# Kernel tuning notes

Measured on AMD Instinct MI355X. Metric: run time of the kernel, lower is better.

Reference implementation:

```python
import jax, jax.numpy as jnp
import numpy as np

N = 50000
E = 1600000
D = 64


def setup_inputs() -> dict:
    key = jax.random.key(0)
    ks = jax.random.split(key, 12)
    glorot = lambda k, shape: jax.random.uniform(
        k, shape, jnp.float32, -1.0, 1.0) * (np.sqrt(2.0) * np.sqrt(6.0 / sum(shape)))
    return {
        "feat": jax.random.normal(ks[0], (N, D), jnp.float32),
        "norm": jax.random.uniform(ks[1], (N,), jnp.float32),
        "edge_src": jax.random.randint(ks[2], (E,), 0, N),
        "edge_dst": jax.random.randint(ks[3], (E,), 0, N),
        "etype": jax.random.randint(ks[4], (E,), 0, 4),
        "W_rel": glorot(ks[5], (D, D)),
        "lin_w": glorot(ks[6], (2 * D, 1)),
        "lin_b": jnp.zeros((1,), jnp.float32),
        "loop_w": glorot(ks[7], (D, D)),
        "evolve_loop_w": glorot(ks[8], (D, D)),
    }


def reference(feat, norm, edge_src, edge_dst, etype, W_rel, lin_w, lin_b,
              loop_w, evolve_loop_w):
    # --- message function: per-edge attention + per-edge matmul ---
    src = feat[edge_src]              # [E, D] gather
    dst = feat[edge_dst]              # [E, D] gather
    att_logit = jnp.concatenate([src, dst], axis=1) @ lin_w + lin_b  # [E, 1]
    atten = jax.nn.sigmoid(jax.nn.relu(att_logit[:, 0]))            # [E]
    # source code applies weight_relation to every edge-type bucket, so the
    # etype split+concat is a no-op permutation of messages
    msg = src @ W_rel                                                # [E, D]

    # --- reduce: attention-weighted mailbox sum (segment reduction) ---
    agg = jax.ops.segment_sum(atten[:, None] * msg, edge_dst, num_segments=N)
    indeg = jax.ops.segment_sum(jnp.ones((edge_dst.shape[0],), feat.dtype),
                                edge_dst, num_segments=N)            # [N]
    has_msg = (indeg > 0)[:, None]
    # DGL: zero in-degree nodes keep their old feat; apply_func scales by norm
    node_feat = jnp.where(has_msg, agg, feat) * norm[:, None]

    # --- self loop: loop_weight where in_degree>0, evolve_loop_weight else ---
    loop_msg = jnp.where(has_msg, feat @ loop_w, feat @ evolve_loop_w)

    return jnp.tanh(node_feat + loop_msg)
```

## Files before the change

kernel.cpp:

```cpp
#include <hip/hip_runtime.h>
#include <hip/hip_bf16.h>
#include <hip/hip_fp16.h>
#include <math.h>


#define D 64
#define SHIFT 6
#define NB (1 << SHIFT)
#define SCM 1024
#define CAPB 2560
#define NPW 8

typedef _Float16 half8 __attribute__((ext_vector_type(8)));
typedef float f32x4 __attribute__((ext_vector_type(4)));

__global__ __launch_bounds__(512) void pre_scatter(
    const float* __restrict__ feat, const float* __restrict__ W_rel,
    const float* __restrict__ lin_w, const float* __restrict__ lin_b,
    const float* __restrict__ loop_w, const float* __restrict__ evolve_w,
    const int* __restrict__ esrc, const int* __restrict__ edst,
    float* __restrict__ s1, float* __restrict__ s2, __half* __restrict__ FWh,
    __half* __restrict__ WT, int* __restrict__ gcur,
    unsigned* __restrict__ ebuf, int N, int E, int C) {
  __shared__ int h[SCM];
  __shared__ int cur[SCM];
  __shared__ int bl[SCM];
  for (int i = threadIdx.x; i < C; i += 512) h[i] = 0;

  if (blockIdx.x == 0) {
    for (int i = threadIdx.x; i < 192 * 64; i += 512) {
      const int c192 = i >> 6, k = i & 63;
      const int m = c192 >> 6, c = c192 & 63;
      const float* Wm = (m == 0) ? W_rel : (m == 1) ? loop_w : evolve_w;
      WT[i] = __float2half(Wm[k * 64 + c]);
    }
  }

  const int lane = threadIdx.x & 63;
  const int w    = threadIdx.x >> 6;
  const int r    = lane & 15;
  const int g    = lane >> 4;
  const int m0   = (blockIdx.x * 8 + w) * 16;
  if (m0 < N) {
    half8 bw[4][2];
    half8 ba[2];
    #pragma unroll
    for (int ks = 0; ks < 2; ++ks) {
      #pragma unroll
      for (int j = 0; j < 8; ++j) {
        const int k = ks * 32 + g * 8 + j;
        #pragma unroll
        for (int nt = 0; nt < 4; ++nt)
          bw[nt][ks][j] = (_Float16)W_rel[k * 64 + nt * 16 + r];
        const float av = (r == 0) ? lin_w[k] : (r == 1) ? lin_w[64 + k] : 0.0f;
        ba[ks][j] = (_Float16)av;
      }
    }

    half8 ah[2], al[2];
    const int arow = m0 + r;
    #pragma unroll
    for (int ks = 0; ks < 2; ++ks) {
      float v[8];
      if (arow < N) {
        const float4 u0 = *(const float4*)&feat[(size_t)arow * D + ks * 32 + g * 8];
        const float4 u1 = *(const float4*)&feat[(size_t)arow * D + ks * 32 + g * 8 + 4];
        v[0] = u0.x; v[1] = u0.y; v[2] = u0.z; v[3] = u0.w;
        v[4] = u1.x; v[5] = u1.y; v[6] = u1.z; v[7] = u1.w;
      } else {
        #pragma unroll
        for (int q = 0; q < 8; ++q) v[q] = 0.0f;
      }
      #pragma unroll
      for (int q = 0; q < 8; ++q) {
        const _Float16 hh = (_Float16)v[q];
        ah[ks][q] = hh;
        al[ks][q] = (_Float16)(v[q] - (float)hh);
      }
    }

    #pragma unroll
    for (int nt = 0; nt < 4; ++nt) {
      f32x4 acc = {0.0f, 0.0f, 0.0f, 0.0f};
      #pragma unroll
      for (int ks = 0; ks < 2; ++ks) {
        acc = __builtin_amdgcn_mfma_f32_16x16x32_f16(ah[ks], bw[nt][ks], acc, 0, 0, 0);
        acc = __builtin_amdgcn_mfma_f32_16x16x32_f16(al[ks], bw[nt][ks], acc, 0, 0, 0);
      }
      #pragma unroll
      for (int q = 0; q < 4; ++q) {
        const int n = m0 + g * 4 + q;
        if (n < N) FWh[(size_t)n * D + nt * 16 + r] = __float2half(acc[q]);
      }
    }

    f32x4 acc5 = {0.0f, 0.0f, 0.0f, 0.0f};
    #pragma unroll
    for (int ks = 0; ks < 2; ++ks) {
      acc5 = __builtin_amdgcn_mfma_f32_16x16x32_f16(ah[ks], ba[ks], acc5, 0, 0, 0);
      acc5 = __builtin_amdgcn_mfma_f32_16x16x32_f16(al[ks], ba[ks], acc5, 0, 0, 0);
    }
    if (r < 2) {
      const float b = lin_b[0];
      #pragma unroll
      for (int q = 0; q < 4; ++q) {
        const int n = m0 + g * 4 + q;
        if (n < N) {
          if (r == 0) s1[n] = acc5[q] + b;
          else        s2[n] = acc5[q];
        }
      }
    }
  }

  __syncthreads();

  const int E4 = E >> 2;
  const int4* edst4 = (const int4*)edst;
  const int4* esrc4 = (const int4*)esrc;
  const int i4 = blockIdx.x * 512 + threadIdx.x;
  const bool tail0 = (blockIdx.x == 0) && (threadIdx.x == 0);

  if (i4 < E4) {
    const int4 d = edst4[i4];
    atomicAdd(&h[d.x >> SHIFT], 1);
    atomicAdd(&h[d.y >> SHIFT], 1);
    atomicAdd(&h[d.z >> SHIFT], 1);
    atomicAdd(&h[d.w >> SHIFT], 1);
  }
  if (tail0) for (int e = E4 << 2; e < E; ++e) atomicAdd(&h[edst[e] >> SHIFT], 1);
  __syncthreads();
  for (int i = threadIdx.x; i < C; i += 512) {
    const int v = h[i];
    bl[i] = v ? atomicAdd(&gcur[i], v) : 0;
    cur[i] = 0;
  }
  __syncthreads();

  if (i4 < E4) {
    const int4 s = esrc4[i4];
    const int4 d = edst4[i4];
    const int ss[4] = {s.x, s.y, s.z, s.w};
    const int dd[4] = {d.x, d.y, d.z, d.w};
    #pragma unroll
    for (int j = 0; j < 4; ++j) {
      const int bk = dd[j] >> SHIFT;
      const int rr = atomicAdd(&cur[bk], 1);
      ebuf[(size_t)bk * CAPB + bl[bk] + rr] =
          (unsigned)ss[j] | ((unsigned)(dd[j] & (NB - 1)) << 26);
    }
  }
  if (tail0) {
    for (int e = E4 << 2; e < E; ++e) {
      const int bk = edst[e] >> SHIFT;
      const int rr = atomicAdd(&cur[bk], 1);
      ebuf[(size_t)bk * CAPB + bl[bk] + rr] =
          (unsigned)esrc[e] | ((unsigned)(edst[e] & (NB - 1)) << 26);
    }
  }
}

__global__ __launch_bounds__(512, 4) void sort_reduce_finalize(
    const float* __restrict__ feat, const __half* __restrict__ FWh,
    const __half* __restrict__ WT, const float* __restrict__ norm,
    const float* __restrict__ s1, const float* __restrict__ s2,
    const int* __restrict__ gcur, const unsigned* __restrict__ ebuf,
    float* __restrict__ out, int C, int N) {
  __shared__ uint2 sdata[CAPB];
  __shared__ float Yl[NB * D];
  __shared__ float s2l[NB];
  __shared__ int hist[NB];
  __shared__ int starts[NB + 1];
  __shared__ int roff[NB];

  const int tid  = threadIdx.x;
  const int lane = tid & 63;
  const int w    = tid >> 6;
  const int b    = blockIdx.x;
  const int n0   = b << SHIFT;
  const int beg  = b * CAPB;
  const int cnt  = min(gcur[b], CAPB);

  if (tid < NB) {
    hist[tid] = 0;
    const int n = n0 + tid;
    s2l[tid] = (n < N) ? s2[n] : 0.0f;
  }
  __syncthreads();

  unsigned ereg[5];
  float    areg[5];
  #pragma unroll
  for (int k = 0; k < 5; ++k) {
    const int i = tid + (k << 9);
    if (i < cnt) {
      ereg[k] = ebuf[beg + i];
      atomicAdd(&hist[ereg[k] >> 26], 1);
    }
  }
  #pragma unroll
  for (int k = 0; k < 5; ++k) {
    const int i = tid + (k << 9);
    if (i < cnt) {
      const unsigned src = ereg[k] & 0x03FFFFFFu;
      const float v = s1[src] + s2l[ereg[k] >> 26];
      areg[k] = 1.0f / (1.0f + __expf(-fmaxf(v, 0.0f)));
    }
  }
  __syncthreads();
  if (tid < 64) {
    const int v = hist[tid];
    int incl = v;
    #pragma unroll
    for (int off = 1; off < 64; off <<= 1) {
      const int o = __shfl_up(incl, off, 64);
      if (tid >= off) incl += o;
    }
    starts[tid] = incl - v;
    roff[tid]   = incl - v;
    if (tid == 63) starts[64] = incl;
  }
  __syncthreads();
  #pragma unroll
  for (int k = 0; k < 5; ++k) {
    const int i = tid + (k << 9);
    if (i < cnt) {
      const int pos = atomicAdd(&roff[ereg[k] >> 26], 1);
      sdata[pos] = make_uint2(ereg[k], __float_as_uint(areg[k]));
    }
  }

  {
    const int r = lane & 15, g = lane >> 4;
    const bool evw = (w >= 4);
    const int mt = w & 3;
    bool skip = false;
    if (evw) {
      const int rr0 = mt * 16;
      const int flag = (lane < 16)
          ? ((starts[rr0 + lane + 1] > starts[rr0 + lane]) ? 1 : 0) : 1;
      skip = (__ballot(flag == 0) == 0ULL);
    }
    if (!skip) {
      half8 ah[2], al[2];
      const int arow = n0 + mt * 16 + r;
      #pragma unroll
      for (int ks = 0; ks < 2; ++ks) {
        float v[8];
        if (arow < N) {
          const float4 u0 = *(const float4*)&feat[(size_t)arow * D + ks * 32 + g * 8];
          const float4 u1 = *(const float4*)&feat[(size_t)arow * D + ks * 32 + g * 8 + 4];
          v[0] = u0.x; v[1] = u0.y; v[2] = u0.z; v[3] = u0.w;
          v[4] = u1.x; v[5] = u1.y; v[6] = u1.z; v[7] = u1.w;
        } else {
          #pragma unroll
          for (int q = 0; q < 8; ++q) v[q] = 0.0f;
        }
        #pragma unroll
        for (int q = 0; q < 8; ++q) {
          const _Float16 hh = (_Float16)v[q];
          ah[ks][q] = hh;
          al[ks][q] = (_Float16)(v[q] - (float)hh);
        }
      }
      const int wrow0 = evw ? 128 : 64;
      #pragma unroll
      for (int nt = 0; nt < 4; ++nt) {
        f32x4 a0 = {0.0f, 0.0f, 0.0f, 0.0f};
        #pragma unroll
        for (int ks = 0; ks < 2; ++ks) {
          const half8 bw = *reinterpret_cast<const half8*>(
              WT + (size_t)(wrow0 + nt * 16 + r) * 64 + ks * 32 + g * 8);
          a0 = __builtin_amdgcn_mfma_f32_16x16x32_f16(ah[ks], bw, a0, 0, 0, 0);
          a0 = __builtin_amdgcn_mfma_f32_16x16x32_f16(al[ks], bw, a0, 0, 0, 0);
        }
        #pragma unroll
        for (int q = 0; q < 4; ++q) {
          const int gr = mt * 16 + g * 4 + q;
          const bool hm = starts[gr + 1] > starts[gr];
          if (evw != hm) Yl[gr * D + nt * 16 + r] = a0[q];
        }
      }
    }
  }
  __syncthreads();

  const int qe = lane >> 4;
  const int qc = lane & 15;
  float agg[NPW];
  #pragma unroll
  for (int j = 0; j < NPW; ++j) agg[j] = 0.0f;
  for (int j = 0; j < NPW; ++j) {
    const int dl = w * NPW + j;
    const int n  = n0 + dl;
    if (n >= N) break;
    const int rb = __builtin_amdgcn_readfirstlane(starts[dl]);
    const int re = __builtin_amdgcn_readfirstlane(starts[dl + 1]);
    float sa = 0.0f, sb = 0.0f, sc = 0.0f, sd = 0.0f;
    int p = rb;
    for (; p + 16 <= re; p += 16) {
      uint2 ee[4];
      #pragma unroll
      for (int q = 0; q < 4; ++q) ee[q] = sdata[p + 4 * q + qe];
      #pragma unroll
      for (int q = 0; q < 4; ++q) {
        const uint2 vv = *(const uint2*)(
            FWh + (((size_t)(ee[q].x & 0x03FFFFFFu)) << 6) + (qc << 2));
        const float a = __uint_as_float(ee[q].y);
        const float2 f0 = __half22float2(*(const __half2*)&vv.x);
        const float2 f1 = __half22float2(*(const __half2*)&vv.y);
        sa += a * f0.x; sb += a * f0.y; sc += a * f1.x; sd += a * f1.y;
      }
    }
    for (; p < re; p += 4) {
      const int idx = p + qe;
      const bool vld = idx < re;
      const uint2 e = sdata[vld ? idx : rb];
      const uint2 vv = *(const uint2*)(
          FWh + (((size_t)(e.x & 0x03FFFFFFu)) << 6) + (qc << 2));
      const float a = vld ? __uint_as_float(e.y) : 0.0f;
      const float2 f0 = __half22float2(*(const __half2*)&vv.x);
      const float2 f1 = __half22float2(*(const __half2*)&vv.y);
      sa += a * f0.x; sb += a * f0.y; sc += a * f1.x; sd += a * f1.y;
    }
    sa += __shfl_xor(sa, 16, 64); sa += __shfl_xor(sa, 32, 64);
    sb += __shfl_xor(sb, 16, 64); sb += __shfl_xor(sb, 32, 64);
    sc += __shfl_xor(sc, 16, 64); sc += __shfl_xor(sc, 32, 64);
    sd += __shfl_xor(sd, 16, 64); sd += __shfl_xor(sd, 32, 64);
    const float t0 = __shfl(sa, lane >> 2, 64);
    const float t1 = __shfl(sb, lane >> 2, 64);
    const float t2 = __shfl(sc, lane >> 2, 64);
    const float t3 = __shfl(sd, lane >> 2, 64);
    const int sel = lane & 3;
    agg[j] = (sel == 0) ? t0 : (sel == 1) ? t1 : (sel == 2) ? t2 : t3;
  }

  for (int j = 0; j < NPW; ++j) {
    const int dl = w * NPW + j;
    const int n  = n0 + dl;
    if (n >= N) break;
    const bool hm = starts[dl + 1] > starts[dl];
    const float nr = norm[n];
    const float base = hm ? agg[j] : feat[(size_t)n * D + lane];
    out[(size_t)n * D + lane] = tanhf(base * nr + Yl[dl * D + lane]);
  }
}

extern "C" void kernel_launch(void* const* d_in, const int* in_sizes, int n_in,
                              void* d_out, int out_size, void* d_ws, size_t ws_size,
                              hipStream_t stream) {
  const float* feat     = (const float*)d_in[0];
  const float* norm     = (const float*)d_in[1];
  const int*   esrc     = (const int*)d_in[2];
  const int*   edst     = (const int*)d_in[3];
  const float* W_rel    = (const float*)d_in[5];
  const float* lin_w    = (const float*)d_in[6];
  const float* lin_b    = (const float*)d_in[7];
  const float* loop_w   = (const float*)d_in[8];
  const float* evolve_w = (const float*)d_in[9];
  float* out = (float*)d_out;

  const int N = in_sizes[1];
  const int E = in_sizes[2];
  const int C = (N + NB - 1) >> SHIFT;

  char* p = (char*)d_ws;
  float*    s1   = (float*)p;    p += (size_t)N * sizeof(float);
  float*    s2   = (float*)p;    p += (size_t)N * sizeof(float);
  int*      gcur = (int*)p;      p += (size_t)2048 * sizeof(int);
  __half*   WT   = (__half*)p;   p += (size_t)192 * 64 * sizeof(__half);
  __half*   FWh  = (__half*)p;   p += (size_t)N * D * sizeof(__half);
  unsigned* ebuf = (unsigned*)p;

  const int E4 = E >> 2;
  const int eblocks = (E4 + 511) / 512;

  hipMemsetAsync(gcur, 0, (size_t)C * sizeof(int), stream);
  pre_scatter<<<eblocks, 512, 0, stream>>>(feat, W_rel, lin_w, lin_b,
                                           loop_w, evolve_w, esrc, edst,
                                           s1, s2, FWh, WT, gcur, ebuf,
                                           N, E, C);
  sort_reduce_finalize<<<C, 512, 0, stream>>>(feat, FWh, WT, norm, s1, s2,
                                              gcur, ebuf, out, C, N);
}
```

Before: 155.4 us.

## Replace bucketed edge scatter and in-block sort with per-node fixed-capacity slots

The edge scatter now appends each edge into a fixed-capacity (80) slot array per destination node, using global atomics on a per-node counter. This replaces the per-block shared-memory histogram, global bucket reservation and the in-block counting sort. The reduce kernel reads each node's slots directly and keeps only per-slot attention in shared memory. This removes several barriers and the shared-memory sort, but it adds contended global atomics and a larger, mostly padded edge buffer. Edges past the cap are silently dropped, so correctness depends on in-degree staying at or below 80, which holds for the random test graph (mean in-degree 32).

```diff
diff --git a/kernel.cpp b/kernel.cpp
--- a/kernel.cpp
+++ b/kernel.cpp
@@ -7,8 +7,7 @@
 #define D 64
 #define SHIFT 6
 #define NB (1 << SHIFT)
-#define SCM 1024
-#define CAPB 2560
+#define CAP 80
 #define NPW 8
 
 typedef _Float16 half8 __attribute__((ext_vector_type(8)));
@@ -20,13 +19,8 @@
     const float* __restrict__ loop_w, const float* __restrict__ evolve_w,
     const int* __restrict__ esrc, const int* __restrict__ edst,
     float* __restrict__ s1, float* __restrict__ s2, __half* __restrict__ FWh,
-    __half* __restrict__ WT, int* __restrict__ gcur,
-    unsigned* __restrict__ ebuf, int N, int E, int C) {
-  __shared__ int h[SCM];
-  __shared__ int cur[SCM];
-  __shared__ int bl[SCM];
-  for (int i = threadIdx.x; i < C; i += 512) h[i] = 0;
-
+    __half* __restrict__ WT, int* __restrict__ ncur,
+    unsigned* __restrict__ ebuf, int N, int E) {
   if (blockIdx.x == 0) {
     for (int i = threadIdx.x; i < 192 * 64; i += 512) {
       const int c192 = i >> 6, k = i & 63;
@@ -113,49 +107,29 @@
     }
   }
 
-  __syncthreads();
-
   const int E4 = E >> 2;
   const int4* edst4 = (const int4*)edst;
   const int4* esrc4 = (const int4*)esrc;
   const int i4 = blockIdx.x * 512 + threadIdx.x;
-  const bool tail0 = (blockIdx.x == 0) && (threadIdx.x == 0);
-
-  if (i4 < E4) {
-    const int4 d = edst4[i4];
-    atomicAdd(&h[d.x >> SHIFT], 1);
-    atomicAdd(&h[d.y >> SHIFT], 1);
-    atomicAdd(&h[d.z >> SHIFT], 1);
-    atomicAdd(&h[d.w >> SHIFT], 1);
-  }
-  if (tail0) for (int e = E4 << 2; e < E; ++e) atomicAdd(&h[edst[e] >> SHIFT], 1);
-  __syncthreads();
-  for (int i = threadIdx.x; i < C; i += 512) {
-    const int v = h[i];
-    bl[i] = v ? atomicAdd(&gcur[i], v) : 0;
-    cur[i] = 0;
-  }
-  __syncthreads();
 
   if (i4 < E4) {
     const int4 s = esrc4[i4];
     const int4 d = edst4[i4];
     const int ss[4] = {s.x, s.y, s.z, s.w};
     const int dd[4] = {d.x, d.y, d.z, d.w};
+    int slot[4];
+    #pragma unroll
+    for (int j = 0; j < 4; ++j) slot[j] = atomicAdd(&ncur[dd[j]], 1);
     #pragma unroll
     for (int j = 0; j < 4; ++j) {
-      const int bk = dd[j] >> SHIFT;
-      const int rr = atomicAdd(&cur[bk], 1);
-      ebuf[(size_t)bk * CAPB + bl[bk] + rr] =
-          (unsigned)ss[j] | ((unsigned)(dd[j] & (NB - 1)) << 26);
-    }
-  }
-  if (tail0) {
+      if (slot[j] < CAP)
+        ebuf[(size_t)dd[j] * CAP + slot[j]] = (unsigned)ss[j];
+    }
+  }
+  if (blockIdx.x == 0 && threadIdx.x == 0) {
     for (int e = E4 << 2; e < E; ++e) {
-      const int bk = edst[e] >> SHIFT;
-      const int rr = atomicAdd(&cur[bk], 1);
-      ebuf[(size_t)bk * CAPB + bl[bk] + rr] =
-          (unsigned)esrc[e] | ((unsigned)(edst[e] & (NB - 1)) << 26);
+      const int slot = atomicAdd(&ncur[edst[e]], 1);
+      if (slot < CAP) ebuf[(size_t)edst[e] * CAP + slot] = (unsigned)esrc[e];
     }
   }
 }
@@ -164,69 +138,36 @@
     const float* __restrict__ feat, const __half* __restrict__ FWh,
     const __half* __restrict__ WT, const float* __restrict__ norm,
     const float* __restrict__ s1, const float* __restrict__ s2,
-    const int* __restrict__ gcur, const unsigned* __restrict__ ebuf,
-    float* __restrict__ out, int C, int N) {
-  __shared__ uint2 sdata[CAPB];
+    const int* __restrict__ ncur, const unsigned* __restrict__ ebuf,
+    float* __restrict__ out, int N) {
+  __shared__ float attL[NB * CAP];
   __shared__ float Yl[NB * D];
   __shared__ float s2l[NB];
-  __shared__ int hist[NB];
-  __shared__ int starts[NB + 1];
-  __shared__ int roff[NB];
+  __shared__ int   cntL[NB];
 
   const int tid  = threadIdx.x;
   const int lane = tid & 63;
   const int w    = tid >> 6;
   const int b    = blockIdx.x;
   const int n0   = b << SHIFT;
-  const int beg  = b * CAPB;
-  const int cnt  = min(gcur[b], CAPB);
+  const size_t rbase = (size_t)n0 * CAP;
 
   if (tid < NB) {
-    hist[tid] = 0;
     const int n = n0 + tid;
-    s2l[tid] = (n < N) ? s2[n] : 0.0f;
+    cntL[tid] = (n < N) ? min(ncur[n], CAP) : 0;
+    s2l[tid]  = (n < N) ? s2[n] : 0.0f;
   }
   __syncthreads();
 
-  unsigned ereg[5];
-  float    areg[5];
   #pragma unroll
-  for (int k = 0; k < 5; ++k) {
+  for (int k = 0; k < (NB * CAP) / 512; ++k) {
     const int i = tid + (k << 9);
-    if (i < cnt) {
-      ereg[k] = ebuf[beg + i];
-      atomicAdd(&hist[ereg[k] >> 26], 1);
-    }
-  }
-  #pragma unroll
-  for (int k = 0; k < 5; ++k) {
-    const int i = tid + (k << 9);
-    if (i < cnt) {
-      const unsigned src = ereg[k] & 0x03FFFFFFu;
-      const float v = s1[src] + s2l[ereg[k] >> 26];
-      areg[k] = 1.0f / (1.0f + __expf(-fmaxf(v, 0.0f)));
-    }
-  }
-  __syncthreads();
-  if (tid < 64) {
-    const int v = hist[tid];
-    int incl = v;
-    #pragma unroll
-    for (int off = 1; off < 64; off <<= 1) {
-      const int o = __shfl_up(incl, off, 64);
-      if (tid >= off) incl += o;
-    }
-    starts[tid] = incl - v;
-    roff[tid]   = incl - v;
-    if (tid == 63) starts[64] = incl;
-  }
-  __syncthreads();
-  #pragma unroll
-  for (int k = 0; k < 5; ++k) {
-    const int i = tid + (k << 9);
-    if (i < cnt) {
-      const int pos = atomicAdd(&roff[ereg[k] >> 26], 1);
-      sdata[pos] = make_uint2(ereg[k], __float_as_uint(areg[k]));
+    const unsigned e = ebuf[rbase + i];
+    const int node = i / CAP;
+    const int slot = i - node * CAP;
+    if (slot < cntL[node]) {
+      const float v = s1[e & 0x03FFFFFFu] + s2l[node];
+      attL[i] = 1.0f / (1.0f + __expf(-fmaxf(v, 0.0f)));
     }
   }
 
@@ -237,8 +178,7 @@
     bool skip = false;
     if (evw) {
       const int rr0 = mt * 16;
-      const int flag = (lane < 16)
-          ? ((starts[rr0 + lane + 1] > starts[rr0 + lane]) ? 1 : 0) : 1;
+      const int flag = (lane < 16) ? ((cntL[rr0 + lane] > 0) ? 1 : 0) : 1;
       skip = (__ballot(flag == 0) == 0ULL);
     }
     if (!skip) {
@@ -269,15 +209,15 @@
         f32x4 a0 = {0.0f, 0.0f, 0.0f, 0.0f};
         #pragma unroll
         for (int ks = 0; ks < 2; ++ks) {
-          const half8 bw = *reinterpret_cast<const half8*>(
+          const half8 bwv = *reinterpret_cast<const half8*>(
               WT + (size_t)(wrow0 + nt * 16 + r) * 64 + ks * 32 + g * 8);
-          a0 = __builtin_amdgcn_mfma_f32_16x16x32_f16(ah[ks], bw, a0, 0, 0, 0);
-          a0 = __builtin_amdgcn_mfma_f32_16x16x32_f16(al[ks], bw, a0, 0, 0, 0);
+          a0 = __builtin_amdgcn_mfma_f32_16x16x32_f16(ah[ks], bwv, a0, 0, 0, 0);
+          a0 = __builtin_amdgcn_mfma_f32_16x16x32_f16(al[ks], bwv, a0, 0, 0, 0);
         }
         #pragma unroll
         for (int q = 0; q < 4; ++q) {
           const int gr = mt * 16 + g * 4 + q;
-          const bool hm = starts[gr + 1] > starts[gr];
+          const bool hm = cntL[gr] > 0;
           if (evw != hm) Yl[gr * D + nt * 16 + r] = a0[q];
         }
       }
@@ -292,33 +232,38 @@
   for (int j = 0; j < NPW; ++j) agg[j] = 0.0f;
   for (int j = 0; j < NPW; ++j) {
     const int dl = w * NPW + j;
-    const int n  = n0 + dl;
-    if (n >= N) break;
-    const int rb = __builtin_amdgcn_readfirstlane(starts[dl]);
-    const int re = __builtin_amdgcn_readfirstlane(starts[dl + 1]);
+    const int cn = cntL[dl];
+    if (cn == 0) continue;
+    const size_t gbase = rbase + (size_t)dl * CAP;
+    const int aoff = dl * CAP;
     float sa = 0.0f, sb = 0.0f, sc = 0.0f, sd = 0.0f;
-    int p = rb;
-    for (; p + 16 <= re; p += 16) {
-      uint2 ee[4];
-      #pragma unroll
-      for (int q = 0; q < 4; ++q) ee[q] = sdata[p + 4 * q + qe];
+    int p = 0;
+    for (; p + 16 <= cn; p += 16) {
+      unsigned ee[4];
+      float    aa[4];
+      #pragma unroll
+      for (int q = 0; q < 4; ++q) {
+        ee[q] = ebuf[gbase + p + 4 * q + qe];
+        aa[q] = attL[aoff + p + 4 * q + qe];
+      }
       #pragma unroll
       for (int q = 0; q < 4; ++q) {
         const uint2 vv = *(const uint2*)(
-            FWh + (((size_t)(ee[q].x & 0x03FFFFFFu)) << 6) + (qc << 2));
-        const float a = __uint_as_float(ee[q].y);
+            FWh + (((size_t)(ee[q] & 0x03FFFFFFu)) << 6) + (qc << 2));
         const float2 f0 = __half22float2(*(const __half2*)&vv.x);
         const float2 f1 = __half22float2(*(const __half2*)&vv.y);
-        sa += a * f0.x; sb += a * f0.y; sc += a * f1.x; sd += a * f1.y;
-      }
-    }
-    for (; p < re; p += 4) {
+        sa += aa[q] * f0.x; sb += aa[q] * f0.y;
+        sc += aa[q] * f1.x; sd += aa[q] * f1.y;
+      }
+    }
+    for (; p < cn; p += 4) {
       const int idx = p + qe;
-      const bool vld = idx < re;
-      const uint2 e = sdata[vld ? idx : rb];
+      const bool vld = idx < cn;
+      const int ridx = vld ? idx : 0;
+      const unsigned e = ebuf[gbase + ridx];
+      const float a = vld ? attL[aoff + ridx] : 0.0f;
       const uint2 vv = *(const uint2*)(
-          FWh + (((size_t)(e.x & 0x03FFFFFFu)) << 6) + (qc << 2));
-      const float a = vld ? __uint_as_float(e.y) : 0.0f;
+          FWh + (((size_t)(e & 0x03FFFFFFu)) << 6) + (qc << 2));
       const float2 f0 = __half22float2(*(const __half2*)&vv.x);
       const float2 f1 = __half22float2(*(const __half2*)&vv.y);
       sa += a * f0.x; sb += a * f0.y; sc += a * f1.x; sd += a * f1.y;
@@ -339,7 +284,7 @@
     const int dl = w * NPW + j;
     const int n  = n0 + dl;
     if (n >= N) break;
-    const bool hm = starts[dl + 1] > starts[dl];
+    const bool hm = cntL[dl] > 0;
     const float nr = norm[n];
     const float base = hm ? agg[j] : feat[(size_t)n * D + lane];
     out[(size_t)n * D + lane] = tanhf(base * nr + Yl[dl * D + lane]);
@@ -367,7 +312,7 @@
   char* p = (char*)d_ws;
   float*    s1   = (float*)p;    p += (size_t)N * sizeof(float);
   float*    s2   = (float*)p;    p += (size_t)N * sizeof(float);
-  int*      gcur = (int*)p;      p += (size_t)2048 * sizeof(int);
+  int*      ncur = (int*)p;      p += (size_t)N * sizeof(int);
   __half*   WT   = (__half*)p;   p += (size_t)192 * 64 * sizeof(__half);
   __half*   FWh  = (__half*)p;   p += (size_t)N * D * sizeof(__half);
   unsigned* ebuf = (unsigned*)p;
@@ -375,11 +320,11 @@
   const int E4 = E >> 2;
   const int eblocks = (E4 + 511) / 512;
 
-  hipMemsetAsync(gcur, 0, (size_t)C * sizeof(int), stream);
+  hipMemsetAsync(ncur, 0, (size_t)N * sizeof(int), stream);
   pre_scatter<<<eblocks, 512, 0, stream>>>(feat, W_rel, lin_w, lin_b,
                                            loop_w, evolve_w, esrc, edst,
-                                           s1, s2, FWh, WT, gcur, ebuf,
-                                           N, E, C);
+                                           s1, s2, FWh, WT, ncur, ebuf,
+                                           N, E);
   sort_reduce_finalize<<<C, 512, 0, stream>>>(feat, FWh, WT, norm, s1, s2,
-                                              gcur, ebuf, out, C, N);
+                                              ncur, ebuf, out, N);
 }
```

Result: slower. 271.9 us (+75.0%).

## Split each destination bucket across two 256-thread blocks handling 32 nodes each

Applied to the files above, without the earlier changes.

The reduce/finalize kernel now launches twice as many blocks of 256 threads, each owning half of a 64-node bucket, selected by bit 31 of the packed edge word. Each block reads the whole bucket's edge list twice (once for the histogram, once for the scatter) and filters to its half. Attention is computed only for its own edges, and shared memory shrinks so more blocks fit per CU. The cost is doubled ebuf reads and a new CAPH overflow cap that silently drops edges beyond 1400 per half.

```diff
diff --git a/kernel.cpp b/kernel.cpp
--- a/kernel.cpp
+++ b/kernel.cpp
@@ -9,6 +9,8 @@
 #define NB (1 << SHIFT)
 #define SCM 1024
 #define CAPB 2560
+#define HN 32
+#define CAPH 1400
 #define NPW 8
 
 typedef _Float16 half8 __attribute__((ext_vector_type(8)));
@@ -160,80 +162,78 @@
   }
 }
 
-__global__ __launch_bounds__(512, 4) void sort_reduce_finalize(
+__global__ __launch_bounds__(256, 8) void sort_reduce_finalize(
     const float* __restrict__ feat, const __half* __restrict__ FWh,
     const __half* __restrict__ WT, const float* __restrict__ norm,
     const float* __restrict__ s1, const float* __restrict__ s2,
     const int* __restrict__ gcur, const unsigned* __restrict__ ebuf,
     float* __restrict__ out, int C, int N) {
-  __shared__ uint2 sdata[CAPB];
-  __shared__ float Yl[NB * D];
-  __shared__ float s2l[NB];
-  __shared__ int hist[NB];
-  __shared__ int starts[NB + 1];
-  __shared__ int roff[NB];
+  __shared__ uint2 sdata[CAPH];
+  __shared__ float Yl[HN * D];
+  __shared__ float s2l[HN];
+  __shared__ int hist[HN];
+  __shared__ int starts[HN + 1];
+  __shared__ int roff[HN];
 
   const int tid  = threadIdx.x;
   const int lane = tid & 63;
   const int w    = tid >> 6;
   const int b    = blockIdx.x;
-  const int n0   = b << SHIFT;
-  const int beg  = b * CAPB;
-  const int cnt  = min(gcur[b], CAPB);
-
-  if (tid < NB) {
+  const int sb   = b >> 1;
+  const unsigned half = (unsigned)(b & 1);
+  const int n0   = b << 5;
+  const int beg  = sb * CAPB;
+  const int cnt  = min(gcur[sb], CAPB);
+
+  if (tid < HN) {
     hist[tid] = 0;
     const int n = n0 + tid;
     s2l[tid] = (n < N) ? s2[n] : 0.0f;
   }
   __syncthreads();
 
-  unsigned ereg[5];
-  float    areg[5];
   #pragma unroll
-  for (int k = 0; k < 5; ++k) {
-    const int i = tid + (k << 9);
+  for (int k = 0; k < 10; ++k) {
+    const int i = tid + (k << 8);
     if (i < cnt) {
-      ereg[k] = ebuf[beg + i];
-      atomicAdd(&hist[ereg[k] >> 26], 1);
-    }
-  }
-  #pragma unroll
-  for (int k = 0; k < 5; ++k) {
-    const int i = tid + (k << 9);
-    if (i < cnt) {
-      const unsigned src = ereg[k] & 0x03FFFFFFu;
-      const float v = s1[src] + s2l[ereg[k] >> 26];
-      areg[k] = 1.0f / (1.0f + __expf(-fmaxf(v, 0.0f)));
-    }
-  }
-  __syncthreads();
-  if (tid < 64) {
+      const unsigned e = ebuf[beg + i];
+      if ((e >> 31) == half) atomicAdd(&hist[(e >> 26) & 31], 1);
+    }
+  }
+  __syncthreads();
+  if (tid < HN) {
     const int v = hist[tid];
     int incl = v;
     #pragma unroll
-    for (int off = 1; off < 64; off <<= 1) {
+    for (int off = 1; off < HN; off <<= 1) {
       const int o = __shfl_up(incl, off, 64);
       if (tid >= off) incl += o;
     }
     starts[tid] = incl - v;
     roff[tid]   = incl - v;
-    if (tid == 63) starts[64] = incl;
+    if (tid == HN - 1) starts[HN] = incl;
   }
   __syncthreads();
   #pragma unroll
-  for (int k = 0; k < 5; ++k) {
-    const int i = tid + (k << 9);
+  for (int k = 0; k < 10; ++k) {
+    const int i = tid + (k << 8);
     if (i < cnt) {
-      const int pos = atomicAdd(&roff[ereg[k] >> 26], 1);
-      sdata[pos] = make_uint2(ereg[k], __float_as_uint(areg[k]));
+      const unsigned e = ebuf[beg + i];
+      if ((e >> 31) == half) {
+        const unsigned src = e & 0x03FFFFFFu;
+        const int nl = (int)((e >> 26) & 31);
+        const float v = s1[src] + s2l[nl];
+        const float att = 1.0f / (1.0f + __expf(-fmaxf(v, 0.0f)));
+        const int pos = atomicAdd(&roff[nl], 1);
+        if (pos < CAPH) sdata[pos] = make_uint2(e, __float_as_uint(att));
+      }
     }
   }
 
   {
     const int r = lane & 15, g = lane >> 4;
-    const bool evw = (w >= 4);
-    const int mt = w & 3;
+    const bool evw = (w >= 2);
+    const int mt = w & 1;
     bool skip = false;
     if (evw) {
       const int rr0 = mt * 16;
@@ -296,7 +296,7 @@
     if (n >= N) break;
     const int rb = __builtin_amdgcn_readfirstlane(starts[dl]);
     const int re = __builtin_amdgcn_readfirstlane(starts[dl + 1]);
-    float sa = 0.0f, sb = 0.0f, sc = 0.0f, sd = 0.0f;
+    float sa = 0.0f, sb2 = 0.0f, sc = 0.0f, sd = 0.0f;
     int p = rb;
     for (; p + 16 <= re; p += 16) {
       uint2 ee[4];
@@ -309,7 +309,7 @@
         const float a = __uint_as_float(ee[q].y);
         const float2 f0 = __half22float2(*(const __half2*)&vv.x);
         const float2 f1 = __half22float2(*(const __half2*)&vv.y);
-        sa += a * f0.x; sb += a * f0.y; sc += a * f1.x; sd += a * f1.y;
+        sa += a * f0.x; sb2 += a * f0.y; sc += a * f1.x; sd += a * f1.y;
       }
     }
     for (; p < re; p += 4) {
@@ -321,14 +321,14 @@
       const float a = vld ? __uint_as_float(e.y) : 0.0f;
       const float2 f0 = __half22float2(*(const __half2*)&vv.x);
       const float2 f1 = __half22float2(*(const __half2*)&vv.y);
-      sa += a * f0.x; sb += a * f0.y; sc += a * f1.x; sd += a * f1.y;
-    }
-    sa += __shfl_xor(sa, 16, 64); sa += __shfl_xor(sa, 32, 64);
-    sb += __shfl_xor(sb, 16, 64); sb += __shfl_xor(sb, 32, 64);
-    sc += __shfl_xor(sc, 16, 64); sc += __shfl_xor(sc, 32, 64);
-    sd += __shfl_xor(sd, 16, 64); sd += __shfl_xor(sd, 32, 64);
+      sa += a * f0.x; sb2 += a * f0.y; sc += a * f1.x; sd += a * f1.y;
+    }
+    sa  += __shfl_xor(sa, 16, 64);  sa  += __shfl_xor(sa, 32, 64);
+    sb2 += __shfl_xor(sb2, 16, 64); sb2 += __shfl_xor(sb2, 32, 64);
+    sc  += __shfl_xor(sc, 16, 64);  sc  += __shfl_xor(sc, 32, 64);
+    sd  += __shfl_xor(sd, 16, 64);  sd  += __shfl_xor(sd, 32, 64);
     const float t0 = __shfl(sa, lane >> 2, 64);
-    const float t1 = __shfl(sb, lane >> 2, 64);
+    const float t1 = __shfl(sb2, lane >> 2, 64);
     const float t2 = __shfl(sc, lane >> 2, 64);
     const float t3 = __shfl(sd, lane >> 2, 64);
     const int sel = lane & 3;
@@ -363,6 +363,7 @@
   const int N = in_sizes[1];
   const int E = in_sizes[2];
   const int C = (N + NB - 1) >> SHIFT;
+  const int C2 = (N + HN - 1) / HN;
 
   char* p = (char*)d_ws;
   float*    s1   = (float*)p;    p += (size_t)N * sizeof(float);
@@ -380,6 +381,6 @@
                                            loop_w, evolve_w, esrc, edst,
                                            s1, s2, FWh, WT, gcur, ebuf,
                                            N, E, C);
-  sort_reduce_finalize<<<C, 512, 0, stream>>>(feat, FWh, WT, norm, s1, s2,
-                                              gcur, ebuf, out, C, N);
+  sort_reduce_finalize<<<C2, 256, 0, stream>>>(feat, FWh, WT, norm, s1, s2,
+                                               gcur, ebuf, out, C, N);
 }
```

Result: no change. 154.2 us (-0.7%).
